# Kernel tuning notes

Measured on AMD Instinct MI355X. Metric: run time of the kernel, lower is better.

## Reference

```python
import jax, jax.numpy as jnp
import numpy as np

N = 50000      # nodes
E = 800000     # directed edges (before self-loops)
IN = 128       # input feature dim
HID = 32       # per-head hidden channels
HEADS = 4
OUT = 16       # output classes
NEG_SLOPE = 0.2


def setup_inputs() -> dict:
    key = jax.random.key(0)
    ks = jax.random.split(key, 14)
    x = jax.random.normal(ks[0], (N, IN), jnp.float32)
    edge_index = jax.random.randint(ks[1], (2, E), 0, N, dtype=jnp.int64)

    def glorot(k, shape):
        fan = shape[0] + shape[-1]
        s = np.sqrt(6.0 / fan).astype(np.float32)
        return jax.random.uniform(k, shape, jnp.float32, -s, s)

    return {
        "x": x,
        "edge_index": edge_index,
        # layer 0: IN -> HEADS*HID
        "W1": glorot(ks[2], (IN, HEADS * HID)),
        "a_src1": glorot(ks[3], (HEADS, HID)),
        "a_dst1": glorot(ks[4], (HEADS, HID)),
        "b1": jnp.zeros((HEADS * HID,), jnp.float32),
        # layer 1: HEADS*HID -> HEADS*HID
        "W2": glorot(ks[5], (HEADS * HID, HEADS * HID)),
        "a_src2": glorot(ks[6], (HEADS, HID)),
        "a_dst2": glorot(ks[7], (HEADS, HID)),
        "b2": jnp.zeros((HEADS * HID,), jnp.float32),
        # layer 2: HEADS*HID -> OUT, heads=1
        "W3": glorot(ks[8], (HEADS * HID, OUT)),
        "a_src3": glorot(ks[9], (1, OUT)),
        "a_dst3": glorot(ks[10], (1, OUT)),
        "b3": jnp.zeros((OUT,), jnp.float32),
    }


def _gat_layer(x, src, dst, W, a_s, a_d, b):
    """One PyG-style GATConv (eval mode). src/dst include self-loops."""
    H, C = a_s.shape
    h = (x @ W).reshape(N, H, C)                       # [N,H,C]
    e_src = jnp.einsum('nhc,hc->nh', h, a_s)           # [N,H]
    e_dst = jnp.einsum('nhc,hc->nh', h, a_d)
    e = jax.nn.leaky_relu(e_src[src] + e_dst[dst], NEG_SLOPE)   # [E',H]
    # segment softmax over incoming edges of each target node
    m = jax.ops.segment_max(e, dst, num_segments=N)    # [N,H]
    p = jnp.exp(e - m[dst])
    denom = jax.ops.segment_sum(p, dst, num_segments=N)
    alpha = p / (denom[dst] + 1e-16)                   # [E',H]
    out = jax.ops.segment_sum(alpha[:, :, None] * h[src], dst, num_segments=N)
    return out.reshape(N, H * C) + b


def reference(x, edge_index, W1, a_src1, a_dst1, b1, W2, a_src2, a_dst2, b2,
              W3, a_src3, a_dst3, b3):
    loops = jnp.arange(N, dtype=edge_index.dtype)
    src = jnp.concatenate([edge_index[0], loops])
    dst = jnp.concatenate([edge_index[1], loops])
    h = jax.nn.relu(_gat_layer(x, src, dst, W1, a_src1, a_dst1, b1))
    h = jax.nn.relu(_gat_layer(h, src, dst, W2, a_src2, a_dst2, b2))
    return _gat_layer(h, src, dst, W3, a_src3, a_dst3, b3)   # [N, OUT]
```

## Files before the change

### kernel.cpp

```cpp
#include <hip/hip_runtime.h>

#define NODES 50000
#define EDGES 800000
#define EPLUS (EDGES + NODES)
#define GEMMBLK 782
#define FILLBLK 3328
#define CHUNKE 2048
#define NRANGE 8
#define RSPAN 6250
#define CAP 64

typedef __attribute__((ext_vector_type(8))) short bf16x8;
typedef __attribute__((ext_vector_type(4))) float f32x4;
typedef __attribute__((ext_vector_type(4))) short short4v;

__device__ __forceinline__ float ld_f(const void* p, int isbf, size_t i) {
    if (isbf) return __uint_as_float(((unsigned)((const unsigned short*)p)[i]) << 16);
    return ((const float*)p)[i];
}
__device__ __forceinline__ int ld_idx(const int* ei, int i64, int elem) {
    int v = i64 ? ei[(size_t)elem * 2] : ei[elem];
    v = v < 0 ? 0 : v;
    return v >= NODES ? NODES - 1 : v;
}
__device__ __forceinline__ unsigned short f2bf(float f) {
    unsigned u = __float_as_uint(f);
    u = u + 0x7FFFu + ((u >> 16) & 1u);
    return (unsigned short)(u >> 16);
}
__device__ __forceinline__ unsigned pack2bf(float a, float b) {
    return (unsigned)f2bf(a) | ((unsigned)f2bf(b) << 16);
}
__device__ __forceinline__ float bflo(unsigned u) { return __uint_as_float(u << 16); }
__device__ __forceinline__ float bfhi(unsigned u) { return __uint_as_float(u & 0xFFFF0000u); }

__device__ __forceinline__ void detect_flags(const unsigned* xw, const int* eiw,
                                             int* sh, int& isbf, int& i64) {
    const int t = threadIdx.x;
    if (t < 2) sh[t] = 0;
    __syncthreads();
    if (t < 256) {
        unsigned lo = xw[t] & 0xFFFFu;
        int e = (int)((lo >> 7) & 0xFF);
        if (lo == 0u || (e >= 90 && e <= 140)) atomicAdd(&sh[0], 1);
    }
    if (t < 64) {
        if (eiw[2 * t + 1] == 0) atomicAdd(&sh[1], 1);
    }
    __syncthreads();
    isbf = sh[0] > 200 ? 1 : 0;
    i64  = sh[1] > 48 ? 1 : 0;
}

#define O_W1 0
#define O_AS1 16384
#define O_AD1 16512
#define O_B1 16640
#define O_W2 16768
#define O_AS2 33152
#define O_AD2 33280
#define O_B2 33408
#define O_W3 33536
#define O_AS3 35584
#define O_AD3 35600
#define O_B3 35616
#define W_TOTAL 35632

#define PB_CNT 196
#define PB_WC 140
#define PB_F1 64
#define PB_F2 64
#define PB_F3 8
#define PREP_GRID (PB_CNT + PB_WC + PB_F1 + PB_F2 + PB_F3)

__global__ __launch_bounds__(256) void k_prep(
        const unsigned* __restrict__ xraw, const int* __restrict__ ei,
        const void* w1, const void* as1, const void* ad1, const void* b1,
        const void* w2, const void* as2, const void* ad2, const void* b2,
        const void* w3, const void* as3, const void* ad3, const void* b3,
        float* __restrict__ Wc, int* __restrict__ cnt,
        unsigned short* __restrict__ W1fh, unsigned short* __restrict__ W1fl,
        unsigned short* __restrict__ W2fh, unsigned short* __restrict__ W2fl,
        unsigned short* __restrict__ W3fh, unsigned short* __restrict__ W3fl) {
    __shared__ int sh[2];
    const int t = threadIdx.x;
    int isbf, i64;
    detect_flags(xraw, ei, sh, isbf, i64);
    (void)i64;

    int b = blockIdx.x;
    if (b < PB_CNT) {
        int i = b * 256 + t;
        if (i < NODES) cnt[i] = 0;
        return;
    }
    b -= PB_CNT;
    if (b < PB_WC) {
        const int f = b * 256 + t;
        if (f < W_TOTAL) {
            const int sz[12] = {16384,128,128,128,16384,128,128,128,2048,16,16,16};
            const void* ps[12] = {w1,as1,ad1,b1,w2,as2,ad2,b2,w3,as3,ad3,b3};
            int off = 0;
#pragma unroll
            for (int s = 0; s < 12; ++s) {
                if (f >= off && f < off + sz[s]) Wc[f] = ld_f(ps[s], isbf, f - off);
                off += sz[s];
            }
        }
        return;
    }
    b -= PB_WC;
    const void* wsrc; unsigned short *fh, *fl; int ncols; int e;
    if (b < PB_F1)                { wsrc = w1; fh = W1fh; fl = W1fl; ncols = 128; e = b * 256 + t; }
    else if (b < PB_F1 + PB_F2)   { wsrc = w2; fh = W2fh; fl = W2fl; ncols = 128; e = (b - PB_F1) * 256 + t; }
    else                          { wsrc = w3; fh = W3fh; fl = W3fl; ncols = 16;  e = (b - PB_F1 - PB_F2) * 256 + t; }
    const int j = e & 7, l = (e >> 3) & 63;
    int nf, kc;
    if (ncols == 128) { nf = (e >> 9) & 7; kc = e >> 12; }
    else              { nf = 0;            kc = (e >> 9) & 3; }
    const int k = kc * 32 + (l >> 4) * 4 + (j & 3) + (j >> 2) * 16;
    const int n = nf * 16 + (l & 15);
    const float v = ld_f(wsrc, isbf, (size_t)k * ncols + n);
    const unsigned short hi = f2bf(v);
    const float res = v - __uint_as_float(((unsigned)hi) << 16);
    fh[e] = hi;
    fl[e] = f2bf(res);
}

__global__ __launch_bounds__(256, 4) void k_fillgemm1(
        const unsigned* __restrict__ xraw, const int* __restrict__ ei,
        const unsigned short* __restrict__ W1fh, const unsigned short* __restrict__ W1fl,
        const float* __restrict__ Wc,
        unsigned short* __restrict__ hout, float* __restrict__ es, float* __restrict__ ed,
        int* __restrict__ cnt, unsigned short* __restrict__ col) {
    __shared__ int sh[2];
    const int t = threadIdx.x;
    int isbf, i64;
    detect_flags(xraw, ei, sh, isbf, i64);

    if (blockIdx.x >= GEMMBLK) {
        const int fb = blockIdx.x - GEMMBLK;
        const int r  = blockIdx.x & 7;
        const int chunk = fb >> 3;
        const int lo = r * RSPAN, hi = lo + RSPAN;
        const int base = chunk * CHUNKE;
#pragma unroll
        for (int it = 0; it < CHUNKE / 256; ++it) {
            const int e = base + it * 256 + t;
            if (e >= EPLUS) continue;
            int s, d;
            if (e < EDGES) {
                d = ld_idx(ei, i64, EDGES + e);
                if (d < lo || d >= hi) continue;
                s = ld_idx(ei, i64, e);
            } else {
                s = d = e - EDGES;
                if (d < lo || d >= hi) continue;
            }
            int slot = atomicAdd(&cnt[d], 1);
            if (slot < CAP) col[d * CAP + slot] = (unsigned short)s;
        }
        return;
    }

    __shared__ unsigned short Ah[4 * 64 * 8];
    __shared__ unsigned short Al[4 * 64 * 8];
    const int rowBase = blockIdx.x * 64;
    const int w = t >> 6, lane = t & 63;

    f32x4 acc[4][2];
#pragma unroll
    for (int mf = 0; mf < 4; ++mf)
#pragma unroll
        for (int nn = 0; nn < 2; ++nn) acc[mf][nn] = (f32x4){0.f, 0.f, 0.f, 0.f};

    for (int kc = 0; kc < 4; ++kc) {
        __syncthreads();
#pragma unroll
        for (int u = 0; u < 2; ++u) {
            const int f = t + 256 * u;
            const int r = f >> 3, c4 = f & 7;
            int gr = rowBase + r; if (gr >= NODES) gr = NODES - 1;
            const int mf = r >> 4;
            const int l  = (r & 15) + 16 * (c4 & 3);
            const int j0 = 4 * (c4 >> 2);
            const int di = (mf * 64 + l) * 8 + j0;
            if (!isbf) {
                float4 v = *(const float4*)((const float*)xraw + (size_t)gr * 128 + kc * 32 + c4 * 4);
                const unsigned short h0 = f2bf(v.x), h1 = f2bf(v.y), h2 = f2bf(v.z), h3 = f2bf(v.w);
                short4v hv = {(short)h0, (short)h1, (short)h2, (short)h3};
                *(short4v*)&Ah[di] = hv;
                short4v lv = {(short)f2bf(v.x - __uint_as_float((unsigned)h0 << 16)),
                              (short)f2bf(v.y - __uint_as_float((unsigned)h1 << 16)),
                              (short)f2bf(v.z - __uint_as_float((unsigned)h2 << 16)),
                              (short)f2bf(v.w - __uint_as_float((unsigned)h3 << 16))};
                *(short4v*)&Al[di] = lv;
            } else {
                short4v v = *(const short4v*)((const unsigned short*)xraw + (size_t)gr * 128 + kc * 32 + c4 * 4);
                *(short4v*)&Ah[di] = v;
            }
        }
        __syncthreads();
        const int nA = 2 * w, nB = 2 * w + 1;
        const bf16x8 bh0 = *(const bf16x8*)(W1fh + (((size_t)kc * 8 + nA) * 64 + lane) * 8);
        const bf16x8 bh1 = *(const bf16x8*)(W1fh + (((size_t)kc * 8 + nB) * 64 + lane) * 8);
        const bf16x8 bl0 = *(const bf16x8*)(W1fl + (((size_t)kc * 8 + nA) * 64 + lane) * 8);
        const bf16x8 bl1 = *(const bf16x8*)(W1fl + (((size_t)kc * 8 + nB) * 64 + lane) * 8);
#pragma unroll
        for (int mf = 0; mf < 4; ++mf) {
            const bf16x8 ah = *(const bf16x8*)&Ah[(mf * 64 + lane) * 8];
            acc[mf][0] = __builtin_amdgcn_mfma_f32_16x16x32_bf16(ah, bh0, acc[mf][0], 0, 0, 0);
            acc[mf][1] = __builtin_amdgcn_mfma_f32_16x16x32_bf16(ah, bh1, acc[mf][1], 0, 0, 0);
            if (!isbf) {
                const bf16x8 al = *(const bf16x8*)&Al[(mf * 64 + lane) * 8];
                acc[mf][0] = __builtin_amdgcn_mfma_f32_16x16x32_bf16(ah, bl0, acc[mf][0], 0, 0, 0);
                acc[mf][1] = __builtin_amdgcn_mfma_f32_16x16x32_bf16(ah, bl1, acc[mf][1], 0, 0, 0);
                acc[mf][0] = __builtin_amdgcn_mfma_f32_16x16x32_bf16(al, bh0, acc[mf][0], 0, 0, 0);
                acc[mf][1] = __builtin_amdgcn_mfma_f32_16x16x32_bf16(al, bh1, acc[mf][1], 0, 0, 0);
            }
        }
    }

    const int colA = 32 * w + (lane & 15), colB = colA + 16;
    const float asA = Wc[O_AS1 + colA], asB = Wc[O_AS1 + colB];
    const float adA = Wc[O_AD1 + colA], adB = Wc[O_AD1 + colB];
    const int g = lane >> 4;
#pragma unroll
    for (int mf = 0; mf < 4; ++mf) {
#pragma unroll
        for (int r = 0; r < 4; ++r) {
            const int row = rowBase + mf * 16 + 4 * g + r;
            const bool ok = row < NODES;
            const float vA = acc[mf][0][r], vB = acc[mf][1][r];
            if (ok) {
                hout[(size_t)row * 128 + colA] = f2bf(vA);
                hout[(size_t)row * 128 + colB] = f2bf(vB);
            }
            float se = vA * asA + vB * asB;
            float sd = vA * adA + vB * adB;
#pragma unroll
            for (int off = 1; off < 16; off <<= 1) {
                se += __shfl_xor(se, off);
                sd += __shfl_xor(sd, off);
            }
            if (ok && (lane & 15) == 0) {
                es[row * 4 + w] = se;
                ed[row * 4 + w] = sd;
            }
        }
    }
}

__global__ __launch_bounds__(256, 4) void k_gemm128(
        const unsigned short* __restrict__ in,
        const unsigned short* __restrict__ Wfh, const unsigned short* __restrict__ Wfl,
        const float* __restrict__ a_s, const float* __restrict__ a_d,
        unsigned short* __restrict__ hout, float* __restrict__ es, float* __restrict__ ed) {
    __shared__ unsigned short Ah[4 * 64 * 8];
    const int t = threadIdx.x;
    const int rowBase = blockIdx.x * 64;
    const int w = t >> 6, lane = t & 63;

    f32x4 acc[4][2];
#pragma unroll
    for (int mf = 0; mf < 4; ++mf)
#pragma unroll
        for (int nn = 0; nn < 2; ++nn) acc[mf][nn] = (f32x4){0.f, 0.f, 0.f, 0.f};

    for (int kc = 0; kc < 4; ++kc) {
        __syncthreads();
#pragma unroll
        for (int u = 0; u < 2; ++u) {
            const int f = t + 256 * u;
            const int r = f >> 3, c4 = f & 7;
            int gr = rowBase + r; if (gr >= NODES) gr = NODES - 1;
            const int di = ((r >> 4) * 64 + (r & 15) + 16 * (c4 & 3)) * 8 + 4 * (c4 >> 2);
            short4v v = *(const short4v*)(in + (size_t)gr * 128 + kc * 32 + c4 * 4);
            *(short4v*)&Ah[di] = v;
        }
        __syncthreads();
        const int nA = 2 * w, nB = 2 * w + 1;
        const bf16x8 bh0 = *(const bf16x8*)(Wfh + (((size_t)kc * 8 + nA) * 64 + lane) * 8);
        const bf16x8 bh1 = *(const bf16x8*)(Wfh + (((size_t)kc * 8 + nB) * 64 + lane) * 8);
        const bf16x8 bl0 = *(const bf16x8*)(Wfl + (((size_t)kc * 8 + nA) * 64 + lane) * 8);
        const bf16x8 bl1 = *(const bf16x8*)(Wfl + (((size_t)kc * 8 + nB) * 64 + lane) * 8);
#pragma unroll
        for (int mf = 0; mf < 4; ++mf) {
            const bf16x8 ah = *(const bf16x8*)&Ah[(mf * 64 + lane) * 8];
            acc[mf][0] = __builtin_amdgcn_mfma_f32_16x16x32_bf16(ah, bh0, acc[mf][0], 0, 0, 0);
            acc[mf][1] = __builtin_amdgcn_mfma_f32_16x16x32_bf16(ah, bh1, acc[mf][1], 0, 0, 0);
            acc[mf][0] = __builtin_amdgcn_mfma_f32_16x16x32_bf16(ah, bl0, acc[mf][0], 0, 0, 0);
            acc[mf][1] = __builtin_amdgcn_mfma_f32_16x16x32_bf16(ah, bl1, acc[mf][1], 0, 0, 0);
        }
    }

    const int colA = 32 * w + (lane & 15), colB = colA + 16;
    const float asA = a_s[colA], asB = a_s[colB];
    const float adA = a_d[colA], adB = a_d[colB];
    const int g = lane >> 4;
#pragma unroll
    for (int mf = 0; mf < 4; ++mf) {
#pragma unroll
        for (int r = 0; r < 4; ++r) {
            const int row = rowBase + mf * 16 + 4 * g + r;
            const bool ok = row < NODES;
            const float vA = acc[mf][0][r], vB = acc[mf][1][r];
            if (ok) {
                hout[(size_t)row * 128 + colA] = f2bf(vA);
                hout[(size_t)row * 128 + colB] = f2bf(vB);
            }
            float se = vA * asA + vB * asB;
            float sd = vA * adA + vB * adB;
#pragma unroll
            for (int off = 1; off < 16; off <<= 1) {
                se += __shfl_xor(se, off);
                sd += __shfl_xor(sd, off);
            }
            if (ok && (lane & 15) == 0) {
                es[row * 4 + w] = se;
                ed[row * 4 + w] = sd;
            }
        }
    }
}

__global__ __launch_bounds__(256, 4) void k_gemm16(
        const unsigned short* __restrict__ in,
        const unsigned short* __restrict__ Wfh, const unsigned short* __restrict__ Wfl,
        const float* __restrict__ a_s, const float* __restrict__ a_d,
        unsigned short* __restrict__ hout, float* __restrict__ es, float* __restrict__ ed) {
    __shared__ unsigned short Ah[4 * 64 * 8];
    const int t = threadIdx.x;
    const int rowBase = blockIdx.x * 64;
    const int w = t >> 6, lane = t & 63;

    f32x4 acc = (f32x4){0.f, 0.f, 0.f, 0.f};

    for (int kc = 0; kc < 4; ++kc) {
        __syncthreads();
#pragma unroll
        for (int u = 0; u < 2; ++u) {
            const int f = t + 256 * u;
            const int r = f >> 3, c4 = f & 7;
            int gr = rowBase + r; if (gr >= NODES) gr = NODES - 1;
            const int di = ((r >> 4) * 64 + (r & 15) + 16 * (c4 & 3)) * 8 + 4 * (c4 >> 2);
            short4v v = *(const short4v*)(in + (size_t)gr * 128 + kc * 32 + c4 * 4);
            *(short4v*)&Ah[di] = v;
        }
        __syncthreads();
        const bf16x8 bh = *(const bf16x8*)(Wfh + ((size_t)kc * 64 + lane) * 8);
        const bf16x8 bl = *(const bf16x8*)(Wfl + ((size_t)kc * 64 + lane) * 8);
        const bf16x8 ah = *(const bf16x8*)&Ah[(w * 64 + lane) * 8];
        acc = __builtin_amdgcn_mfma_f32_16x16x32_bf16(ah, bh, acc, 0, 0, 0);
        acc = __builtin_amdgcn_mfma_f32_16x16x32_bf16(ah, bl, acc, 0, 0, 0);
    }

    const int c = lane & 15, g = lane >> 4;
    const float asv = a_s[c], adv = a_d[c];
#pragma unroll
    for (int r = 0; r < 4; ++r) {
        const int row = rowBase + w * 16 + 4 * g + r;
        const bool ok = row < NODES;
        if (ok) hout[(size_t)row * 16 + c] = f2bf(acc[r]);
        float se = acc[r] * asv;
        float sd = acc[r] * adv;
#pragma unroll
        for (int off = 1; off < 16; off <<= 1) {
            se += __shfl_xor(se, off);
            sd += __shfl_xor(sd, off);
        }
        if (ok && c == 0) { es[row] = se; ed[row] = sd; }
    }
}

__global__ void k_gather4(const int* __restrict__ cnt, const unsigned short* __restrict__ col,
                          const float* __restrict__ es, const float* __restrict__ ed,
                          const unsigned short* __restrict__ hfeat,
                          const float* __restrict__ bias, unsigned short* __restrict__ outb) {
    const int nd = blockIdx.x * 4 + (threadIdx.x >> 6);
    if (nd >= NODES) return;
    const int lane = threadIdx.x & 63;
    int deg = cnt[nd]; deg = deg < CAP ? deg : CAP;
    const int start = nd * CAP;

    const int esub = lane >> 4;
    const int c = lane & 15;
    const int myh = c >> 2;
    const float edh = ed[nd * 4 + myh];
    const uint4* __restrict__ h4 = (const uint4*)hfeat;
    float a[8] = {0.f,0.f,0.f,0.f,0.f,0.f,0.f,0.f};
    float den = 0.f;

    int e = esub;
    for (; e + 4 < deg; e += 8) {
        int s0 = col[start + e];
        int s1 = col[start + e + 4];
        uint4 u0 = h4[(size_t)s0 * 16 + c];
        uint4 u1 = h4[(size_t)s1 * 16 + c];
        float v0 = es[s0 * 4 + myh] + edh; v0 = v0 > 0.f ? v0 : 0.2f * v0;
        float v1 = es[s1 * 4 + myh] + edh; v1 = v1 > 0.f ? v1 : 0.2f * v1;
        float p0 = __expf(v0);
        float p1 = __expf(v1);
        den += p0 + p1;
        a[0] += p0 * bflo(u0.x) + p1 * bflo(u1.x);
        a[1] += p0 * bfhi(u0.x) + p1 * bfhi(u1.x);
        a[2] += p0 * bflo(u0.y) + p1 * bflo(u1.y);
        a[3] += p0 * bfhi(u0.y) + p1 * bfhi(u1.y);
        a[4] += p0 * bflo(u0.z) + p1 * bflo(u1.z);
        a[5] += p0 * bfhi(u0.z) + p1 * bfhi(u1.z);
        a[6] += p0 * bflo(u0.w) + p1 * bflo(u1.w);
        a[7] += p0 * bfhi(u0.w) + p1 * bfhi(u1.w);
    }
    for (; e < deg; e += 4) {
        int s0 = col[start + e];
        uint4 u0 = h4[(size_t)s0 * 16 + c];
        float v0 = es[s0 * 4 + myh] + edh; v0 = v0 > 0.f ? v0 : 0.2f * v0;
        float p0 = __expf(v0);
        den += p0;
        a[0] += p0 * bflo(u0.x);
        a[1] += p0 * bfhi(u0.x);
        a[2] += p0 * bflo(u0.y);
        a[3] += p0 * bfhi(u0.y);
        a[4] += p0 * bflo(u0.z);
        a[5] += p0 * bfhi(u0.z);
        a[6] += p0 * bflo(u0.w);
        a[7] += p0 * bfhi(u0.w);
    }
    den += __shfl_xor(den, 16);
    den += __shfl_xor(den, 32);
#pragma unroll
    for (int j = 0; j < 8; ++j) {
        a[j] += __shfl_xor(a[j], 16);
        a[j] += __shfl_xor(a[j], 32);
    }

    if (esub == 0) {
        const float inv = 1.f / (den + 1e-16f);
        float4 b0 = ((const float4*)bias)[c * 2];
        float4 b1 = ((const float4*)bias)[c * 2 + 1];
        float o0 = a[0]*inv + b0.x, o1 = a[1]*inv + b0.y;
        float o2 = a[2]*inv + b0.z, o3 = a[3]*inv + b0.w;
        float o4 = a[4]*inv + b1.x, o5 = a[5]*inv + b1.y;
        float o6 = a[6]*inv + b1.z, o7 = a[7]*inv + b1.w;
        o0 = o0 > 0.f ? o0 : 0.f;  o1 = o1 > 0.f ? o1 : 0.f;
        o2 = o2 > 0.f ? o2 : 0.f;  o3 = o3 > 0.f ? o3 : 0.f;
        o4 = o4 > 0.f ? o4 : 0.f;  o5 = o5 > 0.f ? o5 : 0.f;
        o6 = o6 > 0.f ? o6 : 0.f;  o7 = o7 > 0.f ? o7 : 0.f;
        uint4 pk = {pack2bf(o0, o1), pack2bf(o2, o3), pack2bf(o4, o5), pack2bf(o6, o7)};
        ((uint4*)outb)[(size_t)nd * 16 + c] = pk;
    }
}

__global__ void k_gather1(const int* __restrict__ cnt, const unsigned short* __restrict__ col,
                          const float* __restrict__ es, const float* __restrict__ ed,
                          const unsigned short* __restrict__ hfeat,
                          const float* __restrict__ bias, float* __restrict__ outf) {
    const int nd = blockIdx.x * 4 + (threadIdx.x >> 6);
    if (nd >= NODES) return;
    const int lane = threadIdx.x & 63;
    int deg = cnt[nd]; deg = deg < CAP ? deg : CAP;
    const int start = nd * CAP;

    const float edv = ed[nd];
    const int esub = lane >> 3;
    const int c = lane & 7;
    const unsigned* __restrict__ h1 = (const unsigned*)hfeat;
    float a0 = 0.f, a1 = 0.f, den = 0.f;

    int e = esub;
    for (; e + 8 < deg; e += 16) {
        int s0 = col[start + e];
        int s1 = col[start + e + 8];
        unsigned u0 = h1[(size_t)s0 * 8 + c];
        unsigned u1 = h1[(size_t)s1 * 8 + c];
        float v0 = es[s0] + edv; v0 = v0 > 0.f ? v0 : 0.2f * v0;
        float v1 = es[s1] + edv; v1 = v1 > 0.f ? v1 : 0.2f * v1;
        float p0 = __expf(v0);
        float p1 = __expf(v1);
        den += p0 + p1;
        a0 += p0 * bflo(u0) + p1 * bflo(u1);
        a1 += p0 * bfhi(u0) + p1 * bfhi(u1);
    }
    for (; e < deg; e += 8) {
        int s0 = col[start + e];
        unsigned u0 = h1[(size_t)s0 * 8 + c];
        float v0 = es[s0] + edv; v0 = v0 > 0.f ? v0 : 0.2f * v0;
        float p0 = __expf(v0);
        den += p0;
        a0 += p0 * bflo(u0);
        a1 += p0 * bfhi(u0);
    }
    den += __shfl_xor(den, 8);  a0 += __shfl_xor(a0, 8);  a1 += __shfl_xor(a1, 8);
    den += __shfl_xor(den, 16); a0 += __shfl_xor(a0, 16); a1 += __shfl_xor(a1, 16);
    den += __shfl_xor(den, 32); a0 += __shfl_xor(a0, 32); a1 += __shfl_xor(a1, 32);
    if (lane < 8) {
        const float inv = 1.f / (den + 1e-16f);
        float2 b = ((const float2*)bias)[c];
        ((float2*)outf)[(size_t)nd * 8 + c] = make_float2(a0 * inv + b.x, a1 * inv + b.y);
    }
}

extern "C" void kernel_launch(void* const* d_in, const int* in_sizes, int n_in,
                              void* d_out, int out_size, void* d_ws, size_t ws_size,
                              hipStream_t stream) {
    const int* ei = (const int*)d_in[1];
    const unsigned* xraw = (const unsigned*)d_in[0];
    float* out = (float*)d_out;

    char* p = (char*)d_ws;
    unsigned short* Xb  = (unsigned short*)p; p += (size_t)NODES * 128 * 2;
    unsigned short* A   = (unsigned short*)p; p += (size_t)NODES * 128 * 2;
    float*          es  = (float*)p;          p += (size_t)NODES * 4 * 4;
    float*          ed  = (float*)p;          p += (size_t)NODES * 4 * 4;
    float*          Wc  = (float*)p;          p += (size_t)W_TOTAL * 4;
    int*            cnt = (int*)p;            p += (size_t)NODES * 4;
    unsigned short* col = (unsigned short*)p; p += (size_t)NODES * CAP * 2;
    unsigned short* W1fh = (unsigned short*)p; p += 16384 * 2;
    unsigned short* W1fl = (unsigned short*)p; p += 16384 * 2;
    unsigned short* W2fh = (unsigned short*)p; p += 16384 * 2;
    unsigned short* W2fl = (unsigned short*)p; p += 16384 * 2;
    unsigned short* W3fh = (unsigned short*)p; p += 2048 * 2;
    unsigned short* W3fl = (unsigned short*)p; p += 2048 * 2;

    k_prep<<<PREP_GRID, 256, 0, stream>>>(
        xraw, ei,
        d_in[2], d_in[3], d_in[4], d_in[5],
        d_in[6], d_in[7], d_in[8], d_in[9],
        d_in[10], d_in[11], d_in[12], d_in[13],
        Wc, cnt, W1fh, W1fl, W2fh, W2fl, W3fh, W3fl);

    k_fillgemm1<<<GEMMBLK + FILLBLK, 256, 0, stream>>>(
        xraw, ei, W1fh, W1fl, Wc, A, es, ed, cnt, col);

    const int ggrid = (NODES + 3) / 4;
    k_gather4<<<ggrid, 256, 0, stream>>>(cnt, col, es, ed, A, Wc + O_B1, Xb);
    k_gemm128<<<GEMMBLK, 256, 0, stream>>>(Xb, W2fh, W2fl, Wc + O_AS2, Wc + O_AD2, A, es, ed);
    k_gather4<<<ggrid, 256, 0, stream>>>(cnt, col, es, ed, A, Wc + O_B2, Xb);
    k_gemm16<<<GEMMBLK, 256, 0, stream>>>(Xb, W3fh, W3fl, Wc + O_AS3, Wc + O_AD3, A, es, ed);
    k_gather1<<<ggrid, 256, 0, stream>>>(cnt, col, es, ed, A, Wc + O_B3, out);
}
```

Before: 253.8 us.

## Fuse layer aggregation with next layer's GEMM via shared-memory tile

Merges the gather/softmax aggregation of layers 1 and 2 with the following GEMM in a single 512-thread kernel. Each block aggregates 64 nodes, writes the bf16 activations straight into an MFMA-friendly LDS layout, and then runs the projection and attention-score epilogue. This removes the global write and re-read of the intermediate activations and two kernel launches. Separate es/ed buffers are added so the fused kernel never overwrites the scores it is still reading. The cost is that aggregation parallelism is coarser (8 nodes per wave in sequence), with more load imbalance and lower occupancy during the gather phase.

```diff
diff --git a/kernel.cpp b/kernel.cpp
--- a/kernel.cpp
+++ b/kernel.cpp
@@ -251,60 +251,135 @@
     }
 }
 
-__global__ __launch_bounds__(256, 4) void k_gemm128(
-        const unsigned short* __restrict__ in,
+__global__ __launch_bounds__(512, 4) void k_gg128(
+        const int* __restrict__ cnt, const unsigned short* __restrict__ col,
+        const float* __restrict__ esi, const float* __restrict__ edi,
+        const unsigned short* __restrict__ hfeat, const float* __restrict__ bias,
         const unsigned short* __restrict__ Wfh, const unsigned short* __restrict__ Wfl,
         const float* __restrict__ a_s, const float* __restrict__ a_d,
-        unsigned short* __restrict__ hout, float* __restrict__ es, float* __restrict__ ed) {
-    __shared__ unsigned short Ah[4 * 64 * 8];
+        unsigned short* __restrict__ hout, float* __restrict__ eso, float* __restrict__ edo) {
+    __shared__ unsigned short X2f[4 * 4 * 64 * 8];
     const int t = threadIdx.x;
+    const int v = t >> 6, lane = t & 63;
     const int rowBase = blockIdx.x * 64;
-    const int w = t >> 6, lane = t & 63;
-
-    f32x4 acc[4][2];
-#pragma unroll
-    for (int mf = 0; mf < 4; ++mf)
-#pragma unroll
-        for (int nn = 0; nn < 2; ++nn) acc[mf][nn] = (f32x4){0.f, 0.f, 0.f, 0.f};
-
+
+    const int esub = lane >> 4;
+    const int c = lane & 15;
+    const int myh = c >> 2;
+    const uint4* __restrict__ h4 = (const uint4*)hfeat;
+    for (int i = 0; i < 8; ++i) {
+        const int r = v * 8 + i;
+        const int nd = rowBase + r;
+        if (nd >= NODES) break;
+        int deg = cnt[nd]; deg = deg < CAP ? deg : CAP;
+        const int start = nd * CAP;
+        const float edh = edi[nd * 4 + myh];
+        float a[8] = {0.f,0.f,0.f,0.f,0.f,0.f,0.f,0.f};
+        float den = 0.f;
+        int e = esub;
+        for (; e + 4 < deg; e += 8) {
+            int s0 = col[start + e];
+            int s1 = col[start + e + 4];
+            uint4 u0 = h4[(size_t)s0 * 16 + c];
+            uint4 u1 = h4[(size_t)s1 * 16 + c];
+            float v0 = esi[s0 * 4 + myh] + edh; v0 = v0 > 0.f ? v0 : 0.2f * v0;
+            float v1 = esi[s1 * 4 + myh] + edh; v1 = v1 > 0.f ? v1 : 0.2f * v1;
+            float p0 = __expf(v0);
+            float p1 = __expf(v1);
+            den += p0 + p1;
+            a[0] += p0 * bflo(u0.x) + p1 * bflo(u1.x);
+            a[1] += p0 * bfhi(u0.x) + p1 * bfhi(u1.x);
+            a[2] += p0 * bflo(u0.y) + p1 * bflo(u1.y);
+            a[3] += p0 * bfhi(u0.y) + p1 * bfhi(u1.y);
+            a[4] += p0 * bflo(u0.z) + p1 * bflo(u1.z);
+            a[5] += p0 * bfhi(u0.z) + p1 * bfhi(u1.z);
+            a[6] += p0 * bflo(u0.w) + p1 * bflo(u1.w);
+            a[7] += p0 * bfhi(u0.w) + p1 * bfhi(u1.w);
+        }
+        for (; e < deg; e += 4) {
+            int s0 = col[start + e];
+            uint4 u0 = h4[(size_t)s0 * 16 + c];
+            float v0 = esi[s0 * 4 + myh] + edh; v0 = v0 > 0.f ? v0 : 0.2f * v0;
+            float p0 = __expf(v0);
+            den += p0;
+            a[0] += p0 * bflo(u0.x);
+            a[1] += p0 * bfhi(u0.x);
+            a[2] += p0 * bflo(u0.y);
+            a[3] += p0 * bfhi(u0.y);
+            a[4] += p0 * bflo(u0.z);
+            a[5] += p0 * bfhi(u0.z);
+            a[6] += p0 * bflo(u0.w);
+            a[7] += p0 * bfhi(u0.w);
+        }
+        den += __shfl_xor(den, 16);
+        den += __shfl_xor(den, 32);
+#pragma unroll
+        for (int j = 0; j < 8; ++j) {
+            a[j] += __shfl_xor(a[j], 16);
+            a[j] += __shfl_xor(a[j], 32);
+        }
+        if (esub == 0) {
+            const float inv = 1.f / (den + 1e-16f);
+            float4 b0 = ((const float4*)bias)[c * 2];
+            float4 b1 = ((const float4*)bias)[c * 2 + 1];
+            float o0 = a[0]*inv + b0.x, o1 = a[1]*inv + b0.y;
+            float o2 = a[2]*inv + b0.z, o3 = a[3]*inv + b0.w;
+            float o4 = a[4]*inv + b1.x, o5 = a[5]*inv + b1.y;
+            float o6 = a[6]*inv + b1.z, o7 = a[7]*inv + b1.w;
+            o0 = o0 > 0.f ? o0 : 0.f;  o1 = o1 > 0.f ? o1 : 0.f;
+            o2 = o2 > 0.f ? o2 : 0.f;  o3 = o3 > 0.f ? o3 : 0.f;
+            o4 = o4 > 0.f ? o4 : 0.f;  o5 = o5 > 0.f ? o5 : 0.f;
+            o6 = o6 > 0.f ? o6 : 0.f;  o7 = o7 > 0.f ? o7 : 0.f;
+            const int cc = c & 3;
+            const int kc = c >> 2;
+            const int mf = r >> 4;
+            const int l0 = (r & 15) + 16 * ((2 * cc) & 3);
+            const int l1 = (r & 15) + 16 * ((2 * cc + 1) & 3);
+            const int j0 = (cc < 2) ? 0 : 4;
+            short4v w0 = {(short)f2bf(o0), (short)f2bf(o1), (short)f2bf(o2), (short)f2bf(o3)};
+            short4v w1 = {(short)f2bf(o4), (short)f2bf(o5), (short)f2bf(o6), (short)f2bf(o7)};
+            *(short4v*)&X2f[((kc * 4 + mf) * 64 + l0) * 8 + j0] = w0;
+            *(short4v*)&X2f[((kc * 4 + mf) * 64 + l1) * 8 + j0] = w1;
+        }
+    }
+    __syncthreads();
+
+    const int vr = v >> 2, vc = v & 3;
+    f32x4 acc[2][2];
+#pragma unroll
+    for (int m = 0; m < 2; ++m)
+#pragma unroll
+        for (int nn = 0; nn < 2; ++nn) acc[m][nn] = (f32x4){0.f, 0.f, 0.f, 0.f};
+
+    const int nA = 2 * vc, nB = 2 * vc + 1;
+#pragma unroll
     for (int kc = 0; kc < 4; ++kc) {
-        __syncthreads();
-#pragma unroll
-        for (int u = 0; u < 2; ++u) {
-            const int f = t + 256 * u;
-            const int r = f >> 3, c4 = f & 7;
-            int gr = rowBase + r; if (gr >= NODES) gr = NODES - 1;
-            const int di = ((r >> 4) * 64 + (r & 15) + 16 * (c4 & 3)) * 8 + 4 * (c4 >> 2);
-            short4v v = *(const short4v*)(in + (size_t)gr * 128 + kc * 32 + c4 * 4);
-            *(short4v*)&Ah[di] = v;
-        }
-        __syncthreads();
-        const int nA = 2 * w, nB = 2 * w + 1;
         const bf16x8 bh0 = *(const bf16x8*)(Wfh + (((size_t)kc * 8 + nA) * 64 + lane) * 8);
         const bf16x8 bh1 = *(const bf16x8*)(Wfh + (((size_t)kc * 8 + nB) * 64 + lane) * 8);
         const bf16x8 bl0 = *(const bf16x8*)(Wfl + (((size_t)kc * 8 + nA) * 64 + lane) * 8);
         const bf16x8 bl1 = *(const bf16x8*)(Wfl + (((size_t)kc * 8 + nB) * 64 + lane) * 8);
 #pragma unroll
-        for (int mf = 0; mf < 4; ++mf) {
-            const bf16x8 ah = *(const bf16x8*)&Ah[(mf * 64 + lane) * 8];
-            acc[mf][0] = __builtin_amdgcn_mfma_f32_16x16x32_bf16(ah, bh0, acc[mf][0], 0, 0, 0);
-            acc[mf][1] = __builtin_amdgcn_mfma_f32_16x16x32_bf16(ah, bh1, acc[mf][1], 0, 0, 0);
-            acc[mf][0] = __builtin_amdgcn_mfma_f32_16x16x32_bf16(ah, bl0, acc[mf][0], 0, 0, 0);
-            acc[mf][1] = __builtin_amdgcn_mfma_f32_16x16x32_bf16(ah, bl1, acc[mf][1], 0, 0, 0);
-        }
-    }
-
-    const int colA = 32 * w + (lane & 15), colB = colA + 16;
+        for (int m = 0; m < 2; ++m) {
+            const int mf = 2 * vr + m;
+            const bf16x8 ah = *(const bf16x8*)&X2f[((kc * 4 + mf) * 64 + lane) * 8];
+            acc[m][0] = __builtin_amdgcn_mfma_f32_16x16x32_bf16(ah, bh0, acc[m][0], 0, 0, 0);
+            acc[m][1] = __builtin_amdgcn_mfma_f32_16x16x32_bf16(ah, bh1, acc[m][1], 0, 0, 0);
+            acc[m][0] = __builtin_amdgcn_mfma_f32_16x16x32_bf16(ah, bl0, acc[m][0], 0, 0, 0);
+            acc[m][1] = __builtin_amdgcn_mfma_f32_16x16x32_bf16(ah, bl1, acc[m][1], 0, 0, 0);
+        }
+    }
+
+    const int colA = 32 * vc + (lane & 15), colB = colA + 16;
     const float asA = a_s[colA], asB = a_s[colB];
     const float adA = a_d[colA], adB = a_d[colB];
     const int g = lane >> 4;
 #pragma unroll
-    for (int mf = 0; mf < 4; ++mf) {
+    for (int m = 0; m < 2; ++m) {
 #pragma unroll
         for (int r = 0; r < 4; ++r) {
-            const int row = rowBase + mf * 16 + 4 * g + r;
+            const int row = rowBase + (2 * vr + m) * 16 + 4 * g + r;
             const bool ok = row < NODES;
-            const float vA = acc[mf][0][r], vB = acc[mf][1][r];
+            const float vA = acc[m][0][r], vB = acc[m][1][r];
             if (ok) {
                 hout[(size_t)row * 128 + colA] = f2bf(vA);
                 hout[(size_t)row * 128 + colB] = f2bf(vB);
@@ -317,137 +392,132 @@
                 sd += __shfl_xor(sd, off);
             }
             if (ok && (lane & 15) == 0) {
-                es[row * 4 + w] = se;
-                ed[row * 4 + w] = sd;
-            }
-        }
-    }
-}
-
-__global__ __launch_bounds__(256, 4) void k_gemm16(
-        const unsigned short* __restrict__ in,
+                eso[row * 4 + vc] = se;
+                edo[row * 4 + vc] = sd;
+            }
+        }
+    }
+}
+
+__global__ __launch_bounds__(512, 4) void k_gg16(
+        const int* __restrict__ cnt, const unsigned short* __restrict__ col,
+        const float* __restrict__ esi, const float* __restrict__ edi,
+        const unsigned short* __restrict__ hfeat, const float* __restrict__ bias,
         const unsigned short* __restrict__ Wfh, const unsigned short* __restrict__ Wfl,
         const float* __restrict__ a_s, const float* __restrict__ a_d,
-        unsigned short* __restrict__ hout, float* __restrict__ es, float* __restrict__ ed) {
-    __shared__ unsigned short Ah[4 * 64 * 8];
+        unsigned short* __restrict__ hout, float* __restrict__ eso, float* __restrict__ edo) {
+    __shared__ unsigned short X2f[4 * 4 * 64 * 8];
     const int t = threadIdx.x;
+    const int v = t >> 6, lane = t & 63;
     const int rowBase = blockIdx.x * 64;
-    const int w = t >> 6, lane = t & 63;
-
-    f32x4 acc = (f32x4){0.f, 0.f, 0.f, 0.f};
-
-    for (int kc = 0; kc < 4; ++kc) {
-        __syncthreads();
-#pragma unroll
-        for (int u = 0; u < 2; ++u) {
-            const int f = t + 256 * u;
-            const int r = f >> 3, c4 = f & 7;
-            int gr = rowBase + r; if (gr >= NODES) gr = NODES - 1;
-            const int di = ((r >> 4) * 64 + (r & 15) + 16 * (c4 & 3)) * 8 + 4 * (c4 >> 2);
-            short4v v = *(const short4v*)(in + (size_t)gr * 128 + kc * 32 + c4 * 4);
-            *(short4v*)&Ah[di] = v;
-        }
-        __syncthreads();
-        const bf16x8 bh = *(const bf16x8*)(Wfh + ((size_t)kc * 64 + lane) * 8);
-        const bf16x8 bl = *(const bf16x8*)(Wfl + ((size_t)kc * 64 + lane) * 8);
-        const bf16x8 ah = *(const bf16x8*)&Ah[(w * 64 + lane) * 8];
-        acc = __builtin_amdgcn_mfma_f32_16x16x32_bf16(ah, bh, acc, 0, 0, 0);
-        acc = __builtin_amdgcn_mfma_f32_16x16x32_bf16(ah, bl, acc, 0, 0, 0);
-    }
-
-    const int c = lane & 15, g = lane >> 4;
-    const float asv = a_s[c], adv = a_d[c];
-#pragma unroll
-    for (int r = 0; r < 4; ++r) {
-        const int row = rowBase + w * 16 + 4 * g + r;
-        const bool ok = row < NODES;
-        if (ok) hout[(size_t)row * 16 + c] = f2bf(acc[r]);
-        float se = acc[r] * asv;
-        float sd = acc[r] * adv;
-#pragma unroll
-        for (int off = 1; off < 16; off <<= 1) {
-            se += __shfl_xor(se, off);
-            sd += __shfl_xor(sd, off);
-        }
-        if (ok && c == 0) { es[row] = se; ed[row] = sd; }
-    }
-}
-
-__global__ void k_gather4(const int* __restrict__ cnt, const unsigned short* __restrict__ col,
-                          const float* __restrict__ es, const float* __restrict__ ed,
-                          const unsigned short* __restrict__ hfeat,
-                          const float* __restrict__ bias, unsigned short* __restrict__ outb) {
-    const int nd = blockIdx.x * 4 + (threadIdx.x >> 6);
-    if (nd >= NODES) return;
-    const int lane = threadIdx.x & 63;
-    int deg = cnt[nd]; deg = deg < CAP ? deg : CAP;
-    const int start = nd * CAP;
 
     const int esub = lane >> 4;
     const int c = lane & 15;
     const int myh = c >> 2;
-    const float edh = ed[nd * 4 + myh];
     const uint4* __restrict__ h4 = (const uint4*)hfeat;
-    float a[8] = {0.f,0.f,0.f,0.f,0.f,0.f,0.f,0.f};
-    float den = 0.f;
-
-    int e = esub;
-    for (; e + 4 < deg; e += 8) {
-        int s0 = col[start + e];
-        int s1 = col[start + e + 4];
-        uint4 u0 = h4[(size_t)s0 * 16 + c];
-        uint4 u1 = h4[(size_t)s1 * 16 + c];
-        float v0 = es[s0 * 4 + myh] + edh; v0 = v0 > 0.f ? v0 : 0.2f * v0;
-        float v1 = es[s1 * 4 + myh] + edh; v1 = v1 > 0.f ? v1 : 0.2f * v1;
-        float p0 = __expf(v0);
-        float p1 = __expf(v1);
-        den += p0 + p1;
-        a[0] += p0 * bflo(u0.x) + p1 * bflo(u1.x);
-        a[1] += p0 * bfhi(u0.x) + p1 * bfhi(u1.x);
-        a[2] += p0 * bflo(u0.y) + p1 * bflo(u1.y);
-        a[3] += p0 * bfhi(u0.y) + p1 * bfhi(u1.y);
-        a[4] += p0 * bflo(u0.z) + p1 * bflo(u1.z);
-        a[5] += p0 * bfhi(u0.z) + p1 * bfhi(u1.z);
-        a[6] += p0 * bflo(u0.w) + p1 * bflo(u1.w);
-        a[7] += p0 * bfhi(u0.w) + p1 * bfhi(u1.w);
-    }
-    for (; e < deg; e += 4) {
-        int s0 = col[start + e];
-        uint4 u0 = h4[(size_t)s0 * 16 + c];
-        float v0 = es[s0 * 4 + myh] + edh; v0 = v0 > 0.f ? v0 : 0.2f * v0;
-        float p0 = __expf(v0);
-        den += p0;
-        a[0] += p0 * bflo(u0.x);
-        a[1] += p0 * bfhi(u0.x);
-        a[2] += p0 * bflo(u0.y);
-        a[3] += p0 * bfhi(u0.y);
-        a[4] += p0 * bflo(u0.z);
-        a[5] += p0 * bfhi(u0.z);
-        a[6] += p0 * bflo(u0.w);
-        a[7] += p0 * bfhi(u0.w);
-    }
-    den += __shfl_xor(den, 16);
-    den += __shfl_xor(den, 32);
-#pragma unroll
-    for (int j = 0; j < 8; ++j) {
-        a[j] += __shfl_xor(a[j], 16);
-        a[j] += __shfl_xor(a[j], 32);
-    }
-
-    if (esub == 0) {
-        const float inv = 1.f / (den + 1e-16f);
-        float4 b0 = ((const float4*)bias)[c * 2];
-        float4 b1 = ((const float4*)bias)[c * 2 + 1];
-        float o0 = a[0]*inv + b0.x, o1 = a[1]*inv + b0.y;
-        float o2 = a[2]*inv + b0.z, o3 = a[3]*inv + b0.w;
-        float o4 = a[4]*inv + b1.x, o5 = a[5]*inv + b1.y;
-        float o6 = a[6]*inv + b1.z, o7 = a[7]*inv + b1.w;
-        o0 = o0 > 0.f ? o0 : 0.f;  o1 = o1 > 0.f ? o1 : 0.f;
-        o2 = o2 > 0.f ? o2 : 0.f;  o3 = o3 > 0.f ? o3 : 0.f;
-        o4 = o4 > 0.f ? o4 : 0.f;  o5 = o5 > 0.f ? o5 : 0.f;
-        o6 = o6 > 0.f ? o6 : 0.f;  o7 = o7 > 0.f ? o7 : 0.f;
-        uint4 pk = {pack2bf(o0, o1), pack2bf(o2, o3), pack2bf(o4, o5), pack2bf(o6, o7)};
-        ((uint4*)outb)[(size_t)nd * 16 + c] = pk;
+    for (int i = 0; i < 8; ++i) {
+        const int r = v * 8 + i;
+        const int nd = rowBase + r;
+        if (nd >= NODES) break;
+        int deg = cnt[nd]; deg = deg < CAP ? deg : CAP;
+        const int start = nd * CAP;
+        const float edh = edi[nd * 4 + myh];
+        float a[8] = {0.f,0.f,0.f,0.f,0.f,0.f,0.f,0.f};
+        float den = 0.f;
+        int e = esub;
+        for (; e + 4 < deg; e += 8) {
+            int s0 = col[start + e];
+            int s1 = col[start + e + 4];
+            uint4 u0 = h4[(size_t)s0 * 16 + c];
+            uint4 u1 = h4[(size_t)s1 * 16 + c];
+            float v0 = esi[s0 * 4 + myh] + edh; v0 = v0 > 0.f ? v0 : 0.2f * v0;
+            float v1 = esi[s1 * 4 + myh] + edh; v1 = v1 > 0.f ? v1 : 0.2f * v1;
+            float p0 = __expf(v0);
+            float p1 = __expf(v1);
+            den += p0 + p1;
+            a[0] += p0 * bflo(u0.x) + p1 * bflo(u1.x);
+            a[1] += p0 * bfhi(u0.x) + p1 * bfhi(u1.x);
+            a[2] += p0 * bflo(u0.y) + p1 * bflo(u1.y);
+            a[3] += p0 * bfhi(u0.y) + p1 * bfhi(u1.y);
+            a[4] += p0 * bflo(u0.z) + p1 * bflo(u1.z);
+            a[5] += p0 * bfhi(u0.z) + p1 * bfhi(u1.z);
+            a[6] += p0 * bflo(u0.w) + p1 * bflo(u1.w);
+            a[7] += p0 * bfhi(u0.w) + p1 * bfhi(u1.w);
+        }
+        for (; e < deg; e += 4) {
+            int s0 = col[start + e];
+            uint4 u0 = h4[(size_t)s0 * 16 + c];
+            float v0 = esi[s0 * 4 + myh] + edh; v0 = v0 > 0.f ? v0 : 0.2f * v0;
+            float p0 = __expf(v0);
+            den += p0;
+            a[0] += p0 * bflo(u0.x);
+            a[1] += p0 * bfhi(u0.x);
+            a[2] += p0 * bflo(u0.y);
+            a[3] += p0 * bfhi(u0.y);
+            a[4] += p0 * bflo(u0.z);
+            a[5] += p0 * bfhi(u0.z);
+            a[6] += p0 * bflo(u0.w);
+            a[7] += p0 * bfhi(u0.w);
+        }
+        den += __shfl_xor(den, 16);
+        den += __shfl_xor(den, 32);
+#pragma unroll
+        for (int j = 0; j < 8; ++j) {
+            a[j] += __shfl_xor(a[j], 16);
+            a[j] += __shfl_xor(a[j], 32);
+        }
+        if (esub == 0) {
+            const float inv = 1.f / (den + 1e-16f);
+            float4 b0 = ((const float4*)bias)[c * 2];
+            float4 b1 = ((const float4*)bias)[c * 2 + 1];
+            float o0 = a[0]*inv + b0.x, o1 = a[1]*inv + b0.y;
+            float o2 = a[2]*inv + b0.z, o3 = a[3]*inv + b0.w;
+            float o4 = a[4]*inv + b1.x, o5 = a[5]*inv + b1.y;
+            float o6 = a[6]*inv + b1.z, o7 = a[7]*inv + b1.w;
+            o0 = o0 > 0.f ? o0 : 0.f;  o1 = o1 > 0.f ? o1 : 0.f;
+            o2 = o2 > 0.f ? o2 : 0.f;  o3 = o3 > 0.f ? o3 : 0.f;
+            o4 = o4 > 0.f ? o4 : 0.f;  o5 = o5 > 0.f ? o5 : 0.f;
+            o6 = o6 > 0.f ? o6 : 0.f;  o7 = o7 > 0.f ? o7 : 0.f;
+            const int cc = c & 3;
+            const int kc = c >> 2;
+            const int mf = r >> 4;
+            const int l0 = (r & 15) + 16 * ((2 * cc) & 3);
+            const int l1 = (r & 15) + 16 * ((2 * cc + 1) & 3);
+            const int j0 = (cc < 2) ? 0 : 4;
+            short4v w0 = {(short)f2bf(o0), (short)f2bf(o1), (short)f2bf(o2), (short)f2bf(o3)};
+            short4v w1 = {(short)f2bf(o4), (short)f2bf(o5), (short)f2bf(o6), (short)f2bf(o7)};
+            *(short4v*)&X2f[((kc * 4 + mf) * 64 + l0) * 8 + j0] = w0;
+            *(short4v*)&X2f[((kc * 4 + mf) * 64 + l1) * 8 + j0] = w1;
+        }
+    }
+    __syncthreads();
+
+    if (v < 4) {
+        f32x4 acc = (f32x4){0.f, 0.f, 0.f, 0.f};
+#pragma unroll
+        for (int kc = 0; kc < 4; ++kc) {
+            const bf16x8 bh = *(const bf16x8*)(Wfh + ((size_t)kc * 64 + lane) * 8);
+            const bf16x8 bl = *(const bf16x8*)(Wfl + ((size_t)kc * 64 + lane) * 8);
+            const bf16x8 ah = *(const bf16x8*)&X2f[((kc * 4 + v) * 64 + lane) * 8];
+            acc = __builtin_amdgcn_mfma_f32_16x16x32_bf16(ah, bh, acc, 0, 0, 0);
+            acc = __builtin_amdgcn_mfma_f32_16x16x32_bf16(ah, bl, acc, 0, 0, 0);
+        }
+        const int cc = lane & 15, g = lane >> 4;
+        const float asv = a_s[cc], adv = a_d[cc];
+#pragma unroll
+        for (int r = 0; r < 4; ++r) {
+            const int row = rowBase + v * 16 + 4 * g + r;
+            const bool ok = row < NODES;
+            if (ok) hout[(size_t)row * 16 + cc] = f2bf(acc[r]);
+            float se = acc[r] * asv;
+            float sd = acc[r] * adv;
+#pragma unroll
+            for (int off = 1; off < 16; off <<= 1) {
+                se += __shfl_xor(se, off);
+                sd += __shfl_xor(sd, off);
+            }
+            if (ok && cc == 0) { eso[row] = se; edo[row] = sd; }
+        }
     }
 }
 
@@ -508,10 +578,10 @@
     float* out = (float*)d_out;
 
     char* p = (char*)d_ws;
-    unsigned short* Xb  = (unsigned short*)p; p += (size_t)NODES * 128 * 2;
-    unsigned short* A   = (unsigned short*)p; p += (size_t)NODES * 128 * 2;
-    float*          es  = (float*)p;          p += (size_t)NODES * 4 * 4;
-    float*          ed  = (float*)p;          p += (size_t)NODES * 4 * 4;
+    unsigned short* h2  = (unsigned short*)p; p += (size_t)NODES * 128 * 2;
+    unsigned short* h1  = (unsigned short*)p; p += (size_t)NODES * 128 * 2;
+    float*          es1 = (float*)p;          p += (size_t)NODES * 4 * 4;
+    float*          ed1 = (float*)p;          p += (size_t)NODES * 4 * 4;
     float*          Wc  = (float*)p;          p += (size_t)W_TOTAL * 4;
     int*            cnt = (int*)p;            p += (size_t)NODES * 4;
     unsigned short* col = (unsigned short*)p; p += (size_t)NODES * CAP * 2;
@@ -521,6 +591,8 @@
     unsigned short* W2fl = (unsigned short*)p; p += 16384 * 2;
     unsigned short* W3fh = (unsigned short*)p; p += 2048 * 2;
     unsigned short* W3fl = (unsigned short*)p; p += 2048 * 2;
+    float*          es2 = (float*)p;          p += (size_t)NODES * 4 * 4;
+    float*          ed2 = (float*)p;          p += (size_t)NODES * 4 * 4;
 
     k_prep<<<PREP_GRID, 256, 0, stream>>>(
         xraw, ei,
@@ -530,12 +602,14 @@
         Wc, cnt, W1fh, W1fl, W2fh, W2fl, W3fh, W3fl);
 
     k_fillgemm1<<<GEMMBLK + FILLBLK, 256, 0, stream>>>(
-        xraw, ei, W1fh, W1fl, Wc, A, es, ed, cnt, col);
-
+        xraw, ei, W1fh, W1fl, Wc, h1, es1, ed1, cnt, col);
+
+    k_gg128<<<GEMMBLK, 512, 0, stream>>>(cnt, col, es1, ed1, h1, Wc + O_B1,
+                                         W2fh, W2fl, Wc + O_AS2, Wc + O_AD2,
+                                         h2, es2, ed2);
+    k_gg16<<<GEMMBLK, 512, 0, stream>>>(cnt, col, es2, ed2, h2, Wc + O_B2,
+                                        W3fh, W3fl, Wc + O_AS3, Wc + O_AD3,
+                                        h1, es1, ed1);
     const int ggrid = (NODES + 3) / 4;
-    k_gather4<<<ggrid, 256, 0, stream>>>(cnt, col, es, ed, A, Wc + O_B1, Xb);
-    k_gemm128<<<GEMMBLK, 256, 0, stream>>>(Xb, W2fh, W2fl, Wc + O_AS2, Wc + O_AD2, A, es, ed);
-    k_gather4<<<ggrid, 256, 0, stream>>>(cnt, col, es, ed, A, Wc + O_B2, Xb);
-    k_gemm16<<<GEMMBLK, 256, 0, stream>>>(Xb, W3fh, W3fl, Wc + O_AS3, Wc + O_AD3, A, es, ed);
-    k_gather1<<<ggrid, 256, 0, stream>>>(cnt, col, es, ed, A, Wc + O_B3, out);
-}
+    k_gather1<<<ggrid, 256, 0, stream>>>(cnt, col, es1, ed1, h1, Wc + O_B3, out);
+}
```

Measured after the change: 247.3 us. -2.5%, faster.
